# Optimization experiments

Hardware: AMD Instinct MI355X
Metric: run time of the kernel (lower is better)

Reference implementation:

```python
import jax, jax.numpy as jnp
import numpy as np

B, T, C, H = 2, 4096, 512, 8
D = C // H          # head_size = 64
FF = 4 * C          # 2048
EPS = 1e-5


def _layernorm(x, g, b):
    mu = jnp.mean(x, axis=-1, keepdims=True)
    var = jnp.mean(jnp.square(x - mu), axis=-1, keepdims=True)
    return (x - mu) * jax.lax.rsqrt(var + EPS) * g + b


def setup_inputs() -> dict:
    key = jax.random.key(0)
    ks = jax.random.split(key, 10)
    s = 0.02
    return {
        "x":  jax.random.normal(ks[0], (B, T, C), dtype=jnp.float32),
        # per-head K/Q/V linears (bias=False) packed as [C, C] = concat over heads
        "Wq": jax.random.normal(ks[1], (C, C), dtype=jnp.float32) * s,
        "Wk": jax.random.normal(ks[2], (C, C), dtype=jnp.float32) * s,
        "Wv": jax.random.normal(ks[3], (C, C), dtype=jnp.float32) * s,
        "Wo": jax.random.normal(ks[4], (C, C), dtype=jnp.float32) * s,
        "bo": jnp.zeros((C,), dtype=jnp.float32),
        "W1": jax.random.normal(ks[5], (C, FF), dtype=jnp.float32) * s,
        "b1": jnp.zeros((FF,), dtype=jnp.float32),
        "W2": jax.random.normal(ks[6], (FF, C), dtype=jnp.float32) * s,
        "b2": jnp.zeros((C,), dtype=jnp.float32),
        "g1": jnp.ones((C,), dtype=jnp.float32),
        "be1": jnp.zeros((C,), dtype=jnp.float32),
        "g2": jnp.ones((C,), dtype=jnp.float32),
        "be2": jnp.zeros((C,), dtype=jnp.float32),
    }


def reference(x, Wq, Wk, Wv, Wo, bo, W1, b1, W2, b2, g1, be1, g2, be2):
    # --- self-attention on ln1(x), residual add ---
    h = _layernorm(x, g1, be1)                              # [B,T,C]
    q = (h @ Wq).reshape(B, T, H, D)
    k = (h @ Wk).reshape(B, T, H, D)
    v = (h @ Wv).reshape(B, T, H, D)
    # NOTE: original scales by C**-0.5 (n_embd), NOT head_size**-0.5
    scores = jnp.einsum("bthd,bshd->bhts", q, k) * (C ** -0.5)  # [B,H,T,T]
    causal = jnp.tril(jnp.ones((T, T), dtype=bool))
    scores = jnp.where(causal, scores, -jnp.inf)
    wei = jax.nn.softmax(scores, axis=-1)                   # dropout = identity (eval)
    attn = jnp.einsum("bhts,bshd->bthd", wei, v).reshape(B, T, C)
    x = x + (attn @ Wo + bo)                                # proj dropout = identity
    # --- feed-forward on ln2(x), residual add ---
    h2 = _layernorm(x, g2, be2)
    ff = jax.nn.relu(h2 @ W1 + b1) @ W2 + b2                # dropout = identity
    return x + ff
```

## Files before the change

kernel.cpp:

```cpp
#include <hip/hip_runtime.h>

typedef __attribute__((ext_vector_type(8))) __bf16 bf16x8;
typedef __attribute__((ext_vector_type(4))) __bf16 bf16x4;
typedef __attribute__((ext_vector_type(4))) float f32x4;
typedef __attribute__((ext_vector_type(4))) unsigned int u32x4;
typedef __attribute__((ext_vector_type(4))) unsigned short u16x4;
typedef __attribute__((ext_vector_type(8))) unsigned short u16x8;
typedef __attribute__((ext_vector_type(4))) short s16x4;
typedef unsigned short u16;

static __device__ __forceinline__ u16 f2b(float f) {
    unsigned u = __builtin_bit_cast(unsigned, f);
    u = (u + 0x7FFFu + ((u >> 16) & 1u)) >> 16;
    return (u16)u;
}
static __device__ __forceinline__ float b2f(u16 u) {
    return __builtin_bit_cast(float, ((unsigned)u) << 16);
}
static __device__ __forceinline__ float fexp2(float x) {
#if __has_builtin(__builtin_amdgcn_exp2f)
    return __builtin_amdgcn_exp2f(x);
#else
    return exp2f(x);
#endif
}
static __device__ __forceinline__ f32x4 mfma16(bf16x4 a, bf16x4 b, f32x4 c) {
#if __has_builtin(__builtin_amdgcn_mfma_f32_16x16x16_bf16)
    return __builtin_amdgcn_mfma_f32_16x16x16_bf16(a, b, c, 0, 0, 0);
#else
    return __builtin_amdgcn_mfma_f32_16x16x16bf16_1k(
        __builtin_bit_cast(s16x4, a), __builtin_bit_cast(s16x4, b), c, 0, 0, 0);
#endif
}

static __device__ __forceinline__ void gload16(const u16* g, u16* l) {
    __builtin_amdgcn_global_load_lds(
        (const __attribute__((address_space(1))) unsigned int*)g,
        (__attribute__((address_space(3))) unsigned int*)l, 16, 0, 0);
}

__global__ __launch_bounds__(256) void prep_w(
    const float* __restrict__ Wq, const float* __restrict__ Wk,
    const float* __restrict__ Wv, const float* __restrict__ Wo,
    const float* __restrict__ W1, const float* __restrict__ W2,
    u16* __restrict__ WqkvT, u16* __restrict__ WoT,
    u16* __restrict__ W1T, u16* __restrict__ W2T)
{
    const int i = blockIdx.x;
    const float* src; u16* dst; int K, N, nt, kt;
    if (i < 1024) {
        const int z = i >> 8, idx = i & 255;
        K = 512; N = 512; nt = (idx & 15) * 32; kt = (idx >> 4) * 32;
        if (z == 0)      { src = Wq; dst = WqkvT; }
        else if (z == 1) { src = Wk; dst = WqkvT + 512*512; }
        else if (z == 2) { src = Wv; dst = WqkvT + 1024*512; }
        else             { src = Wo; dst = WoT; }
    } else if (i < 2048) {
        const int idx = i - 1024;
        src = W1; dst = W1T; K = 512; N = 2048;
        nt = (idx & 63) * 32; kt = (idx >> 6) * 32;
    } else {
        const int idx = i - 2048;
        src = W2; dst = W2T; K = 2048; N = 512;
        nt = (idx & 15) * 32; kt = (idx >> 4) * 32;
    }
    __shared__ float tile[32][33];
    const int tx = threadIdx.x & 31, ty = threadIdx.x >> 5;
    #pragma unroll
    for (int r = 0; r < 4; ++r)
        tile[ty + r*8][tx] = src[(size_t)(kt + ty + r*8) * N + nt + tx];
    __syncthreads();
    #pragma unroll
    for (int r = 0; r < 4; ++r)
        dst[(size_t)(nt + ty + r*8) * K + kt + tx] = f2b(tile[tx][ty + r*8]);
}

__global__ __launch_bounds__(256) void ln_rows(
    const float* __restrict__ x, const float* __restrict__ g,
    const float* __restrict__ b, u16* __restrict__ out)
{
    const int row = blockIdx.x * 4 + (threadIdx.x >> 6);
    const int lane = threadIdx.x & 63;
    const float* xr = x + (size_t)row * 512;
    f32x4 v0 = *(const f32x4*)(xr + lane * 4);
    f32x4 v1 = *(const f32x4*)(xr + 256 + lane * 4);
    float s = v0[0]+v0[1]+v0[2]+v0[3]+v1[0]+v1[1]+v1[2]+v1[3];
    #pragma unroll
    for (int o = 1; o < 64; o <<= 1) s += __shfl_xor(s, o);
    const float mu = s * (1.0f / 512.0f);
    float s2 = 0.f;
    #pragma unroll
    for (int i = 0; i < 4; ++i) { float d0 = v0[i]-mu, d1 = v1[i]-mu; s2 += d0*d0 + d1*d1; }
    #pragma unroll
    for (int o = 1; o < 64; o <<= 1) s2 += __shfl_xor(s2, o);
    const float inv = rsqrtf(s2 * (1.0f/512.0f) + 1e-5f);
    f32x4 g0 = *(const f32x4*)(g + lane*4), g1 = *(const f32x4*)(g + 256 + lane*4);
    f32x4 b0 = *(const f32x4*)(b + lane*4), b1 = *(const f32x4*)(b + 256 + lane*4);
    u16x4 p0, p1;
    #pragma unroll
    for (int i = 0; i < 4; ++i) {
        p0[i] = f2b((v0[i]-mu)*inv*g0[i] + b0[i]);
        p1[i] = f2b((v1[i]-mu)*inv*g1[i] + b1[i]);
    }
    u16* orow = out + (size_t)row * 512;
    *(u16x4*)(orow + lane*4)       = p0;
    *(u16x4*)(orow + 256 + lane*4) = p1;
}

template<int FLAGS, int NB, int GX>
__global__ __launch_bounds__(256) void gemm_bt(
    const u16* __restrict__ A, const u16* __restrict__ BT,
    const int N, const int K,
    const float* __restrict__ bias, const float* __restrict__ res,
    void* __restrict__ outv, u16* __restrict__ vt)
{
    constexpr int RING = (NB == 2) ? 3 : 4;
    __shared__ __attribute__((aligned(16))) u16 As[RING * 4096];
    __shared__ __attribute__((aligned(16))) u16 Bs[RING * 2048 * NB];
    const int fid = blockIdx.x;
    const int xcd = fid & 7, s8 = fid >> 3;
    const int colb = s8 % GX, rl = s8 / GX;
    const int m0 = (xcd*8 + rl) << 7;
    const int n0 = colb * (64 * NB);
    const int tid = threadIdx.x, lane = tid & 63, w = tid >> 6;
    const int wr2 = w >> 1, wc = w & 1;
    const int g = lane >> 4, c = lane & 15;
    const f32x4 fz = {0.f, 0.f, 0.f, 0.f};

    f32x4 acc[4][2 * NB];
    #pragma unroll
    for (int m = 0; m < 4; ++m)
      #pragma unroll
      for (int n = 0; n < 2 * NB; ++n) acc[m][n] = fz;

    const int srow = tid >> 2;
    const int scs = (((tid & 3) ^ (srow & 3)) * 8);
    const u16* Ag = A  + (size_t)(m0 + srow)*K + scs;
    const u16* Bg = BT + (size_t)(n0 + srow)*K + scs;
    const size_t rstep = (size_t)64 * K;

    const int nkt = K >> 5;
    auto stage = [&](int slot, int kt) {
        const int k0 = kt << 5;
        u16* ad = &As[0] + slot*4096 + w*512;
        gload16(Ag + k0,         ad);
        gload16(Ag + rstep + k0, ad + 2048);
        u16* bd = &Bs[0] + slot*2048*NB + w*512;
        gload16(Bg + k0, bd);
        if constexpr (NB == 2) gload16(Bg + rstep + k0, bd + 2048);
    };
    stage(0, 0);
    stage(1, (1 < nkt) ? 1 : 0);
    if constexpr (RING == 4) stage(2, (2 < nkt) ? 2 : 0);

    for (int kt = 0; kt < nkt; ++kt) {
        if constexpr (NB == 2) asm volatile("s_waitcnt vmcnt(4)" ::: "memory");
        else                   asm volatile("s_waitcnt vmcnt(6)" ::: "memory");
        __builtin_amdgcn_s_barrier();
        asm volatile("" ::: "memory");
        {
            int tp = kt + RING - 1; if (tp >= nkt) tp = nkt - 1;
            int sl = kt + RING - 1; sl -= (sl / RING) * RING;
            stage(sl, tp);
        }
        const int rd = kt - (kt / RING) * RING;
        const u16* Ab = &As[0] + rd*4096;
        const u16* Bb = &Bs[0] + rd*2048*NB;
        bf16x8 af[4], bfr[2 * NB];
        #pragma unroll
        for (int m = 0; m < 4; ++m) {
            const int row = wr2*64 + m*16 + c;
            af[m] = *(const bf16x8*)(Ab + row*32 + (((g*16) ^ ((row&3)<<4)) >> 1));
        }
        #pragma unroll
        for (int n = 0; n < 2 * NB; ++n) {
            const int row = wc*(32*NB) + n*16 + c;
            bfr[n] = *(const bf16x8*)(Bb + row*32 + (((g*16) ^ ((row&3)<<4)) >> 1));
        }
        #pragma unroll
        for (int m = 0; m < 4; ++m)
          #pragma unroll
          for (int n = 0; n < 2 * NB; ++n)
            acc[m][n] = __builtin_amdgcn_mfma_f32_16x16x32_bf16(af[m], bfr[n], acc[m][n], 0, 0, 0);
    }

    #pragma unroll
    for (int m = 0; m < 4; ++m) {
        const int row = m0 + wr2*64 + m*16 + 4*g;
        #pragma unroll
        for (int n = 0; n < 2 * NB; ++n) {
            const int col = n0 + wc*(32*NB) + n*16 + c;
            const float bv = (FLAGS & 1) ? bias[col] : 0.0f;
            float vv[4];
            #pragma unroll
            for (int r = 0; r < 4; ++r) {
                float v = acc[m][n][r] + bv;
                if (FLAGS & 16) v *= (col < 512) ? 0.0637587246f : 1.0f;
                if (FLAGS & 2) v += res[(size_t)(row + r)*N + col];
                if (FLAGS & 4) v = fmaxf(v, 0.0f);
                vv[r] = v;
            }
            if ((FLAGS & 32) && col >= 1024) {
                u16x4 pv;
                #pragma unroll
                for (int r = 0; r < 4; ++r) pv[r] = f2b(vv[r]);
                *(u16x4*)(vt + (size_t)((row >> 12)*512 + (col - 1024))*4096
                             + (row & 4095)) = pv;
            } else if (FLAGS & 8) {
                #pragma unroll
                for (int r = 0; r < 4; ++r)
                    ((float*)outv)[(size_t)(row + r)*N + col] = vv[r];
            } else {
                #pragma unroll
                for (int r = 0; r < 4; ++r)
                    ((u16*)outv)[(size_t)(row + r)*N + col] = f2b(vv[r]);
            }
        }
    }
}

__global__ __launch_bounds__(256, 3) void attn_fwd(
    const u16* __restrict__ qkv, const u16* __restrict__ vT,
    u16* __restrict__ part, u16* __restrict__ att)
{
    const int fid = blockIdx.x + 160 * blockIdx.y;
    const int xcd = fid & 7, s0i = fid >> 3;
    const int half = (s0i >= 160) ? 1 : 0;
    const int bh = xcd*2 + half, b = bh >> 3, h = bh & 7;
    const int i = 159 - (s0i - half*160);
    int qt, cch, nch;
    if (i < 16)      { qt = i;                         cch = 0;          nch = 1; }
    else if (i < 48) { int j = i-16; qt = 16 + (j>>1); cch = j & 1;      nch = 2; }
    else if (i < 96) { int j = i-48; int d3 = j/3; qt = 32 + d3; cch = j - 3*d3; nch = 3; }
    else             { int j = i-96; qt = 48 + (j>>2); cch = j & 3;      nch = 4; }
    const int ntl = qt + 1;
    const int t0 = (cch * ntl) / nch;
    const int t1 = ((cch + 1) * ntl) / nch;
    const int single = (nch == 1);

    const int tid = threadIdx.x, lane = tid & 63, w = tid >> 6;
    const int g = lane >> 4, c16 = lane & 15;
    __shared__ __attribute__((aligned(16))) u16 smem[24576 + 512];
    u16* Wb = smem + w*6144;
    float* lbuf = (float*)(smem + 24576);

    const u16* qp  = qkv + (size_t)b*4096*1536 + h*64;
    const u16* kp  = qp + 512;
    const u16* vtp = vT + (size_t)bh*64*4096;

    const u16* kgA = kp + (size_t)(16*w + (lane>>3))*1536
                        + (((lane&7) ^ ((lane>>3)&7)) * 8);
    const u16* kgB = kgA + (size_t)8*1536;
    const int sd = lane >> 1;
    const u16* vgA = vtp + (size_t)sd*4096 + 16*w + (((lane&1) ^ ((sd>>2)&1)) * 8);
    const u16* vgB = vgA + (size_t)32*4096;

    const int kOff0 = c16*64 + ((g ^ (c16&7)) * 8);
    const int kOff1 = c16*64 + (((4+g) ^ (c16&7)) * 8);
    const int vroff = c16*16 + (((g>>1) ^ ((c16>>2)&1)) * 8) + (g&1)*4;

    const int Q0 = qt*64;
    bf16x8 qB[4][2];
    #pragma unroll
    for (int sub = 0; sub < 4; ++sub) {
        const u16* qr = qp + (size_t)(Q0 + sub*16 + c16)*1536 + g*8;
        qB[sub][0] = *(const bf16x8*)(qr);
        qB[sub][1] = *(const bf16x8*)(qr + 32);
    }

    const f32x4 fz = {0.f,0.f,0.f,0.f};
    f32x4 oacc[4][4];
    #pragma unroll
    for (int dt = 0; dt < 4; ++dt)
      #pragma unroll
      for (int sub = 0; sub < 4; ++sub) oacc[dt][sub] = fz;
    float lsum[4] = {0.f, 0.f, 0.f, 0.f};

    {
        const int tp1 = (t0+1 < t1) ? (t0+1) : (t1-1);
        u16* sl0 = Wb + (t0 % 3)*2048;
        const size_t ko0 = (size_t)(t0 << 6)*1536; const int kv0 = t0 << 6;
        gload16(kgA + ko0, sl0);        gload16(kgB + ko0, sl0 + 512);
        gload16(vgA + kv0, sl0 + 1024); gload16(vgB + kv0, sl0 + 1536);
        u16* sl1 = Wb + (tp1 % 3)*2048;
        const size_t ko1 = (size_t)(tp1 << 6)*1536; const int kv1 = tp1 << 6;
        gload16(kgA + ko1, sl1);        gload16(kgB + ko1, sl1 + 512);
        gload16(vgA + kv1, sl1 + 1024); gload16(vgB + kv1, sl1 + 1536);
    }
    int rd = t0 % 3;
    int wrs = rd + 2; if (wrs >= 3) wrs -= 3;

    for (int t = t0; t < t1; ++t) {
        {
            const int tp = (t+2 < t1) ? (t+2) : (t1-1);
            u16* slotW = Wb + wrs*2048;
            const size_t ko = (size_t)(tp << 6)*1536; const int kv = tp << 6;
            gload16(kgA + ko, slotW);        gload16(kgB + ko, slotW + 512);
            gload16(vgA + kv, slotW + 1024); gload16(vgB + kv, slotW + 1536);
        }
        asm volatile("s_waitcnt vmcnt(8)" ::: "memory");
        const u16* slotR = Wb + rd*2048;
        const bf16x8 kc0 = *(const bf16x8*)(slotR + kOff0);
        const bf16x8 kc1 = *(const bf16x8*)(slotR + kOff1);
        bf16x4 va[4];
        #pragma unroll
        for (int dt = 0; dt < 4; ++dt)
            va[dt] = *(const bf16x4*)(slotR + 1024 + dt*256 + vroff);
        f32x4 s[4];
        #pragma unroll
        for (int sub = 0; sub < 4; ++sub) {
            f32x4 sv = __builtin_amdgcn_mfma_f32_16x16x32_bf16(kc0, qB[sub][0], fz, 0, 0, 0);
            s[sub]   = __builtin_amdgcn_mfma_f32_16x16x32_bf16(kc1, qB[sub][1], sv, 0, 0, 0);
        }
        bf16x4 pt[4];
        if (t < qt) {
            #pragma unroll
            for (int sub = 0; sub < 4; ++sub) {
                float p0 = fexp2(s[sub][0]), p1 = fexp2(s[sub][1]);
                float p2 = fexp2(s[sub][2]), p3 = fexp2(s[sub][3]);
                lsum[sub] += (p0 + p1) + (p2 + p3);
                bf16x4 pv;
                pv[0] = (__bf16)p0; pv[1] = (__bf16)p1;
                pv[2] = (__bf16)p2; pv[3] = (__bf16)p3;
                pt[sub] = pv;
            }
        } else {
            const int kvbase = t*64 + 16*w + 4*g;
            #pragma unroll
            for (int sub = 0; sub < 4; ++sub) {
                const int qi = Q0 + sub*16 + c16;
                bf16x4 pv; float a = 0.f;
                #pragma unroll
                for (int r = 0; r < 4; ++r) {
                    float p = (kvbase + r <= qi) ? fexp2(s[sub][r]) : 0.0f;
                    a += p; pv[r] = (__bf16)p;
                }
                lsum[sub] += a; pt[sub] = pv;
            }
        }
        #pragma unroll
        for (int dt = 0; dt < 4; ++dt)
          #pragma unroll
          for (int sub = 0; sub < 4; ++sub)
            oacc[dt][sub] = mfma16(va[dt], pt[sub], oacc[dt][sub]);
        rd  = (rd  == 2) ? 0 : rd  + 1;
        wrs = (wrs == 2) ? 0 : wrs + 1;
    }

    #pragma unroll
    for (int sub = 0; sub < 4; ++sub) {
        float v = lsum[sub];
        v += __shfl_xor(v, 16);
        v += __shfl_xor(v, 32);
        if (g == 0) lbuf[w*64 + sub*16 + c16] = v;
    }
    __syncthreads();
    float ltot[4];
    #pragma unroll
    for (int sub = 0; sub < 4; ++sub) {
        const int qr = sub*16 + c16;
        ltot[sub] = lbuf[qr] + lbuf[64 + qr] + lbuf[128 + qr] + lbuf[192 + qr];
    }

    float* img = (float*)smem;
    f32x4 ofin[4];
    const int roff = (g ^ (c16 & 3))*4;
    #pragma unroll
    for (int dt = 0; dt < 4; ++dt) {
        #pragma unroll
        for (int sub = 0; sub < 4; ++sub)
            *(f32x4*)(img + w*1024 + (sub*16 + c16)*16 + roff) = oacc[dt][sub];
        __syncthreads();
        if (w == dt) {
            #pragma unroll
            for (int sub = 0; sub < 4; ++sub) {
                const int off = (sub*16 + c16)*16 + roff;
                f32x4 a0 = *(const f32x4*)(img + off);
                f32x4 a1 = *(const f32x4*)(img + 1024 + off);
                f32x4 a2 = *(const f32x4*)(img + 2048 + off);
                f32x4 a3 = *(const f32x4*)(img + 3072 + off);
                ofin[sub] = (a0 + a1) + (a2 + a3);
            }
        }
        __syncthreads();
    }

    const int dbase = 16*w + 4*g;
    if (single) {
        #pragma unroll
        for (int sub = 0; sub < 4; ++sub) {
            const int qrow = sub*16 + c16;
            const float inv = 1.0f / ltot[sub];
            const f32x4 o = ofin[sub];
            u16x4 ov;
            ov[0] = f2b(o[0]*inv); ov[1] = f2b(o[1]*inv);
            ov[2] = f2b(o[2]*inv); ov[3] = f2b(o[3]*inv);
            *(u16x4*)(att + (size_t)(b*4096 + Q0 + qrow)*512 + h*64 + dbase) = ov;
        }
    } else {
        u16* onum = part + (size_t)(bh*160 + i) * 4224;
        float* lout = (float*)(onum + 4096);
        #pragma unroll
        for (int sub = 0; sub < 4; ++sub) {
            const int qrow = sub*16 + c16;
            const f32x4 o = ofin[sub];
            u16x4 ov;
            ov[0] = f2b(o[0]); ov[1] = f2b(o[1]);
            ov[2] = f2b(o[2]); ov[3] = f2b(o[3]);
            *(u16x4*)(onum + qrow*64 + dbase) = ov;
            if (w == 0 && g == 0) lout[qrow] = ltot[sub];
        }
    }
}

__global__ __launch_bounds__(256) void attn_merge(
    const u16* __restrict__ part, u16* __restrict__ att)
{
    const int qt = 16 + blockIdx.x, bh = blockIdx.y, b = bh >> 3, h = bh & 7;
    int start, n;
    if (qt < 32)      { start = 16 + 2*(qt-16); n = 2; }
    else if (qt < 48) { start = 48 + 3*(qt-32); n = 3; }
    else              { start = 96 + 4*(qt-48); n = 4; }
    const int t = threadIdx.x;
    const int row = t >> 2, c0 = (t & 3) * 16;
    float acc[16];
    #pragma unroll
    for (int j = 0; j < 16; ++j) acc[j] = 0.f;
    float lt = 0.f;
    const u16* p0 = part + (size_t)(bh*160 + start) * 4224;
    for (int ci = 0; ci < n; ++ci) {
        const u16* pc = p0 + (size_t)ci * 4224;
        lt += ((const float*)(pc + 4096))[row];
        u16x8 a = *(const u16x8*)(pc + row*64 + c0);
        u16x8 bq = *(const u16x8*)(pc + row*64 + c0 + 8);
        #pragma unroll
        for (int j = 0; j < 8; ++j) { acc[j] += b2f(a[j]); acc[8+j] += b2f(bq[j]); }
    }
    const float inv = 1.0f / lt;
    u16x8 o1, o2;
    #pragma unroll
    for (int j = 0; j < 8; ++j) { o1[j] = f2b(acc[j]*inv); o2[j] = f2b(acc[8+j]*inv); }
    u16* dst = att + (size_t)(b*4096 + qt*64 + row)*512 + h*64 + c0;
    *(u16x8*)dst = o1;
    *(u16x8*)(dst + 8) = o2;
}

extern "C" void kernel_launch(void* const* d_in, const int* in_sizes, int n_in,
                              void* d_out, int out_size, void* d_ws, size_t ws_size,
                              hipStream_t stream)
{
    (void)in_sizes; (void)n_in; (void)out_size; (void)ws_size;
    const float* x   = (const float*)d_in[0];
    const float* Wq  = (const float*)d_in[1];
    const float* Wk  = (const float*)d_in[2];
    const float* Wv  = (const float*)d_in[3];
    const float* Wo  = (const float*)d_in[4];
    const float* bo  = (const float*)d_in[5];
    const float* W1  = (const float*)d_in[6];
    const float* b1  = (const float*)d_in[7];
    const float* W2  = (const float*)d_in[8];
    const float* b2  = (const float*)d_in[9];
    const float* g1  = (const float*)d_in[10];
    const float* be1 = (const float*)d_in[11];
    const float* g2  = (const float*)d_in[12];
    const float* be2 = (const float*)d_in[13];

    char* ws = (char*)d_ws;
    u16*   WqkvT = (u16*)(ws + 0);
    u16*   WoT   = (u16*)(ws + 1572864);
    u16*   W1T   = (u16*)(ws + 2097152);
    u16*   W2T   = (u16*)(ws + 4194304);
    u16*   H     = (u16*)(ws + 6291456);
    u16*   PART  = (u16*)(ws + 6291456);
    float* X2    = (float*)(ws + 14680064);
    u16*   QKV   = (u16*)(ws + 31457280);
    u16*   VT    = (u16*)(ws + 56623104);
    u16*   ATT   = (u16*)(ws + 65011712);
    u16*   F1    = (u16*)(ws + 31457280);

    prep_w<<<3072, 256, 0, stream>>>(Wq, Wk, Wv, Wo, W1, W2,
                                     WqkvT, WoT, W1T, W2T);
    ln_rows<<<2048, 256, 0, stream>>>(x, g1, be1, H);
    gemm_bt<48, 2, 12><<<768, 256, 0, stream>>>(H, WqkvT, 1536, 512,
                                                nullptr, nullptr, QKV, VT);
    attn_fwd<<<dim3(160, 16), 256, 0, stream>>>(QKV, VT, PART, ATT);
    attn_merge<<<dim3(48, 16), 256, 0, stream>>>(PART, ATT);
    gemm_bt<11, 1, 8><<<512, 256, 0, stream>>>(ATT, WoT, 512, 512,
                                               bo, x, X2, nullptr);
    ln_rows<<<2048, 256, 0, stream>>>(X2, g2, be2, H);
    gemm_bt<5, 2, 16><<<1024, 256, 0, stream>>>(H, W1T, 2048, 512,
                                                b1, nullptr, F1, nullptr);
    gemm_bt<11, 1, 8><<<512, 256, 0, stream>>>(F1, W2T, 512, 2048,
                                               b2, X2, (float*)d_out, nullptr);
}
```

Baseline: 196.0 us.

## Shrink attention LDS to double-buffered V and triple-buffered K for 4 blocks/CU

The attention kernel's shared-memory ring is split so K keeps three slots while V is only double-buffered and prefetched one tile ahead. This cuts LDS per block from about 50KB to 40KB, and launch bounds move from 3 to 4 blocks per CU. The epilogue reduction image is re-laid out with a padded 20-float row stride, and the row-sum buffer is placed after the image region. The trade-off is a shallower prefetch for V and a tighter register budget at 4 waves per SIMD, which could cause spills.

```diff
diff --git a/kernel.cpp b/kernel.cpp
--- a/kernel.cpp
+++ b/kernel.cpp
@@ -219,7 +219,7 @@
     }
 }
 
-__global__ __launch_bounds__(256, 3) void attn_fwd(
+__global__ __launch_bounds__(256, 4) void attn_fwd(
     const u16* __restrict__ qkv, const u16* __restrict__ vT,
     u16* __restrict__ part, u16* __restrict__ att)
 {
@@ -240,9 +240,9 @@
 
     const int tid = threadIdx.x, lane = tid & 63, w = tid >> 6;
     const int g = lane >> 4, c16 = lane & 15;
-    __shared__ __attribute__((aligned(16))) u16 smem[24576 + 512];
-    u16* Wb = smem + w*6144;
-    float* lbuf = (float*)(smem + 24576);
+    __shared__ __attribute__((aligned(16))) u16 smem[20480];
+    u16* Wb = smem + w*5120;
+    float* lbuf = (float*)smem + 5120;
 
     const u16* qp  = qkv + (size_t)b*4096*1536 + h*64;
     const u16* kp  = qp + 512;
@@ -277,35 +277,39 @@
     float lsum[4] = {0.f, 0.f, 0.f, 0.f};
 
     {
+        const int kv0 = t0 << 6;
+        u16* vd = Wb + 3072 + (t0 & 1)*1024;
+        gload16(vgA + kv0, vd); gload16(vgB + kv0, vd + 512);
+        u16* kd = Wb + (t0 % 3)*1024;
+        const size_t ko0 = (size_t)kv0 * 1536;
+        gload16(kgA + ko0, kd); gload16(kgB + ko0, kd + 512);
         const int tp1 = (t0+1 < t1) ? (t0+1) : (t1-1);
-        u16* sl0 = Wb + (t0 % 3)*2048;
-        const size_t ko0 = (size_t)(t0 << 6)*1536; const int kv0 = t0 << 6;
-        gload16(kgA + ko0, sl0);        gload16(kgB + ko0, sl0 + 512);
-        gload16(vgA + kv0, sl0 + 1024); gload16(vgB + kv0, sl0 + 1536);
-        u16* sl1 = Wb + (tp1 % 3)*2048;
-        const size_t ko1 = (size_t)(tp1 << 6)*1536; const int kv1 = tp1 << 6;
-        gload16(kgA + ko1, sl1);        gload16(kgB + ko1, sl1 + 512);
-        gload16(vgA + kv1, sl1 + 1024); gload16(vgB + kv1, sl1 + 1536);
-    }
-    int rd = t0 % 3;
-    int wrs = rd + 2; if (wrs >= 3) wrs -= 3;
+        u16* kd1 = Wb + ((t0+1) % 3)*1024;
+        const size_t ko1 = (size_t)(tp1 << 6)*1536;
+        gload16(kgA + ko1, kd1); gload16(kgB + ko1, kd1 + 512);
+    }
+    int krd = t0 % 3;
+    int kwr = krd + 2; if (kwr >= 3) kwr -= 3;
 
     for (int t = t0; t < t1; ++t) {
         {
-            const int tp = (t+2 < t1) ? (t+2) : (t1-1);
-            u16* slotW = Wb + wrs*2048;
-            const size_t ko = (size_t)(tp << 6)*1536; const int kv = tp << 6;
-            gload16(kgA + ko, slotW);        gload16(kgB + ko, slotW + 512);
-            gload16(vgA + kv, slotW + 1024); gload16(vgB + kv, slotW + 1536);
-        }
-        asm volatile("s_waitcnt vmcnt(8)" ::: "memory");
-        const u16* slotR = Wb + rd*2048;
-        const bf16x8 kc0 = *(const bf16x8*)(slotR + kOff0);
-        const bf16x8 kc1 = *(const bf16x8*)(slotR + kOff1);
+            const int tpv = (t+1 < t1) ? (t+1) : (t1-1);
+            u16* vd = Wb + 3072 + ((t+1) & 1)*1024;
+            gload16(vgA + (tpv << 6), vd); gload16(vgB + (tpv << 6), vd + 512);
+            const int tpk = (t+2 < t1) ? (t+2) : (t1-1);
+            u16* kd = Wb + kwr*1024;
+            const size_t ko = (size_t)(tpk << 6)*1536;
+            gload16(kgA + ko, kd); gload16(kgB + ko, kd + 512);
+        }
+        asm volatile("s_waitcnt vmcnt(6)" ::: "memory");
+        const u16* Kb  = Wb + krd*1024;
+        const u16* Vbp = Wb + 3072 + (t & 1)*1024;
+        const bf16x8 kc0 = *(const bf16x8*)(Kb + kOff0);
+        const bf16x8 kc1 = *(const bf16x8*)(Kb + kOff1);
         bf16x4 va[4];
         #pragma unroll
         for (int dt = 0; dt < 4; ++dt)
-            va[dt] = *(const bf16x4*)(slotR + 1024 + dt*256 + vroff);
+            va[dt] = *(const bf16x4*)(Vbp + dt*256 + vroff);
         f32x4 s[4];
         #pragma unroll
         for (int sub = 0; sub < 4; ++sub) {
@@ -343,8 +347,8 @@
           #pragma unroll
           for (int sub = 0; sub < 4; ++sub)
             oacc[dt][sub] = mfma16(va[dt], pt[sub], oacc[dt][sub]);
-        rd  = (rd  == 2) ? 0 : rd  + 1;
-        wrs = (wrs == 2) ? 0 : wrs + 1;
+        krd = (krd == 2) ? 0 : krd + 1;
+        kwr = (kwr == 2) ? 0 : kwr + 1;
     }
 
     #pragma unroll
@@ -352,33 +356,39 @@
         float v = lsum[sub];
         v += __shfl_xor(v, 16);
         v += __shfl_xor(v, 32);
-        if (g == 0) lbuf[w*64 + sub*16 + c16] = v;
-    }
+        lsum[sub] = v;
+    }
+
+    asm volatile("s_waitcnt vmcnt(0)" ::: "memory");
     __syncthreads();
-    float ltot[4];
-    #pragma unroll
-    for (int sub = 0; sub < 4; ++sub) {
-        const int qr = sub*16 + c16;
-        ltot[sub] = lbuf[qr] + lbuf[64 + qr] + lbuf[128 + qr] + lbuf[192 + qr];
-    }
+    #pragma unroll
+    for (int sub = 0; sub < 4; ++sub)
+        if (g == 0) lbuf[w*64 + sub*16 + c16] = lsum[sub];
 
     float* img = (float*)smem;
     f32x4 ofin[4];
-    const int roff = (g ^ (c16 & 3))*4;
+    float ltot[4];
     #pragma unroll
     for (int dt = 0; dt < 4; ++dt) {
         #pragma unroll
         for (int sub = 0; sub < 4; ++sub)
-            *(f32x4*)(img + w*1024 + (sub*16 + c16)*16 + roff) = oacc[dt][sub];
+            *(f32x4*)(img + w*1280 + (sub*16 + c16)*20 + g*4) = oacc[dt][sub];
         __syncthreads();
+        if (dt == 0) {
+            #pragma unroll
+            for (int sub = 0; sub < 4; ++sub) {
+                const int qr = sub*16 + c16;
+                ltot[sub] = lbuf[qr] + lbuf[64 + qr] + lbuf[128 + qr] + lbuf[192 + qr];
+            }
+        }
         if (w == dt) {
             #pragma unroll
             for (int sub = 0; sub < 4; ++sub) {
-                const int off = (sub*16 + c16)*16 + roff;
+                const int off = (sub*16 + c16)*20 + g*4;
                 f32x4 a0 = *(const f32x4*)(img + off);
-                f32x4 a1 = *(const f32x4*)(img + 1024 + off);
-                f32x4 a2 = *(const f32x4*)(img + 2048 + off);
-                f32x4 a3 = *(const f32x4*)(img + 3072 + off);
+                f32x4 a1 = *(const f32x4*)(img + 1280 + off);
+                f32x4 a2 = *(const f32x4*)(img + 2560 + off);
+                f32x4 a3 = *(const f32x4*)(img + 3840 + off);
                 ofin[sub] = (a0 + a1) + (a2 + a3);
             }
         }
```

Measured after the change: 358.1 us. 1.83x slower.
